# Optimization experiments

Measured on AMD Instinct MI355X. Metric: run time of the kernel, lower is better.

The kernel has to match this reference:

```python
import jax, jax.numpy as jnp
import numpy as np

D_MODEL = 128
D_Q = 16
N_HEADS = 8
LEN_Q = 64
N_LAYERS = 2
F_DIM = 2048
GEST_F_DIM = 512
NUM_GEST = 16
T_FRAMES = 4096
LN_EPS = 1e-5


def _ln(x):
    # fresh nn.LayerNorm(d_model) each call in the torch code -> weight=1, bias=0
    m = jnp.mean(x, axis=-1, keepdims=True)
    v = jnp.var(x, axis=-1, keepdims=True)
    return (x - m) * jax.lax.rsqrt(v + LN_EPS)


def _mha(q_in, k_in, v_in, Wq, Wk, Wv, n_heads, d_q):
    # torch MultiHeadAttention_COG: note self.fc is defined but NOT applied;
    # output = context, then LayerNorm(context + residual)
    B, lq, _ = q_in.shape
    lk = k_in.shape[1]
    Q = (q_in @ Wq).reshape(B, lq, n_heads, d_q).transpose(0, 2, 1, 3)  # [B,h,lq,dq]
    K = (k_in @ Wk).reshape(B, lk, n_heads, d_q).transpose(0, 2, 1, 3)
    V = (v_in @ Wv).reshape(B, lk, n_heads, d_q).transpose(0, 2, 1, 3)
    scores = jnp.einsum('bhqd,bhkd->bhqk', Q, K) / jnp.sqrt(jnp.asarray(d_q, q_in.dtype))
    attn = jax.nn.softmax(scores, axis=-1)
    ctx = jnp.einsum('bhqk,bhkd->bhqd', attn, V)
    ctx = ctx.transpose(0, 2, 1, 3).reshape(B, lq, n_heads * d_q)
    return _ln(ctx + q_in)


def _ffn(x, W1, W2):
    # PoswiseFeedForwardNet: Linear->ReLU->Linear (bias=False), residual + fresh LN
    return _ln(jax.nn.relu(x @ W1) @ W2 + x)


def setup_inputs() -> dict:
    key = jax.random.key(0)
    ks = jax.random.split(key, 12)
    s = 0.02
    inp = {
        'g': jax.random.normal(ks[0], (1, NUM_GEST, GEST_F_DIM), jnp.float32),
        'long_feature': jax.random.normal(ks[1], (1, T_FRAMES, F_DIM), jnp.float32),
        'W_vis': jax.random.normal(ks[2], (F_DIM, D_MODEL), jnp.float32) * s,
        'W_txt': jax.random.normal(ks[3], (GEST_F_DIM, D_MODEL), jnp.float32) * s,
        'Wq_enc': jax.random.normal(ks[4], (N_LAYERS, D_MODEL, N_HEADS * D_Q), jnp.float32) * s,
        'Wk_enc': jax.random.normal(ks[5], (N_LAYERS, D_MODEL, N_HEADS * D_Q), jnp.float32) * s,
        'Wv_enc': jax.random.normal(ks[6], (N_LAYERS, D_MODEL, N_HEADS * D_Q), jnp.float32) * s,
        'W1_ffn': jax.random.normal(ks[7], (N_LAYERS, D_MODEL, F_DIM), jnp.float32) * s,
        'W2_ffn': jax.random.normal(ks[8], (N_LAYERS, F_DIM, D_MODEL), jnp.float32) * s,
        'Wq_f': jax.random.normal(ks[9], (D_MODEL, D_MODEL), jnp.float32) * s,
        'Wk_f': jax.random.normal(ks[10], (D_MODEL, D_MODEL), jnp.float32) * s,
        'Wv_f': jax.random.normal(ks[11], (D_MODEL, D_MODEL), jnp.float32) * s,
    }
    return inp


def reference(g, long_feature, W_vis, W_txt, Wq_enc, Wk_enc, Wv_enc,
              W1_ffn, W2_ffn, Wq_f, Wk_f, Wv_f):
    visual = long_feature[0] @ W_vis           # [T, d_model]
    text = g[0] @ W_txt                        # [num_gest, d_model]
    T = visual.shape[0]

    # per-frame causal window of length LEN_Q with zero left-padding (vectorized)
    padded = jnp.concatenate(
        [jnp.zeros((LEN_Q - 1, D_MODEL), visual.dtype), visual], axis=0)
    idx = jnp.arange(T)[:, None] + jnp.arange(LEN_Q)[None, :]  # [T, len_q]
    visual_feas = padded[idx]                                   # [T, len_q, d_model]
    text_feas = jnp.broadcast_to(text[None], (T, NUM_GEST, D_MODEL))

    # Encoder_COG: normalize visual once, then 2 cross-attn layers (Q=text, K=V=visual)
    vis = _ln(visual_feas)
    t = text_feas
    for l in range(N_LAYERS):
        tq = _ln(t)                                   # norm1
        t = _mha(tq, vis, vis, Wq_enc[l], Wk_enc[l], Wv_enc[l], N_HEADS, D_Q)
        t = _ffn(_ln(t), W1_ffn[l], W2_ffn[l])        # norm3 then FFN

    # final single-head attention: Q=enc_outputs, K=V=text, d_q=d_model
    dec = _mha(t, text_feas, text_feas, Wq_f, Wk_f, Wv_f, 1, D_MODEL)  # [T,num_gest,d_model]
    return dec.reshape(T, -1)[None]  # [1, T, num_gest*d_model]
```

## Files before the change

kernel.cpp:

```cpp
#include <hip/hip_runtime.h>
#include <math.h>

#define TFRAMES 4096
#define DM 128
#define LQ 64
#define NG 16
#define NH 8
#define DQH 16
#define FD 2048
#define GFD 512
#define PAD 63
#define KVROWS (TFRAMES + PAD)
#define ASTRIDE (KVROWS * DM)
#define FPB 4
#define MROWS (FPB * NG)
#define STS 136
#define VTS 72
#define PBS 72
#define UROWS (LQ + FPB - 1)

#define OFF_WVH  0
#define OFF_WVL  131072
#define OFF_WKVH 262144
#define OFF_WKVL 294912
#define OFF_KV   (TFRAMES * DM)
#define OFF_TEXT (OFF_KV + 2 * ASTRIDE)
#define OFF_KF   (OFF_TEXT + NG * DM)
#define OFF_VF   (OFF_KF + NG * DM)
#define OFF_W1T  (OFF_VF + NG * DM)
#define OFF_W2T  (OFF_W1T + 262144)
#define OFF_WQT  (OFF_W2T + 262144)
#define OFF_WQFT (OFF_WQT + 16384)

typedef __attribute__((ext_vector_type(8))) short bf16x8;
typedef __attribute__((ext_vector_type(4))) float f32x4;
#define MFMA16(a, b, c) __builtin_amdgcn_mfma_f32_16x16x32_bf16(a, b, c, 0, 0, 0)

__device__ __forceinline__ short bfc(float x) {
    union { float f; unsigned u; } v; v.f = x;
    unsigned r = v.u + 0x7fffu + ((v.u >> 16) & 1u);
    return (short)(r >> 16);
}
__device__ __forceinline__ float b2f(short s) {
    union { unsigned u; float f; } v;
    v.u = ((unsigned)(unsigned short)s) << 16;
    return v.f;
}
__device__ __forceinline__ bf16x8 shiftf(int4 a, int4 b, int f) {
    const int wo = f >> 1;
    const int sh = (f & 1) * 16;
    int w0 = wo ? a.y : a.x;
    int w1 = wo ? a.z : a.y;
    int w2 = wo ? a.w : a.z;
    int w3 = wo ? b.x : a.w;
    int w4 = wo ? b.y : b.x;
    int o0 = __builtin_amdgcn_alignbit(w1, w0, sh);
    int o1 = __builtin_amdgcn_alignbit(w2, w1, sh);
    int o2 = __builtin_amdgcn_alignbit(w3, w2, sh);
    int o3 = __builtin_amdgcn_alignbit(w4, w3, sh);
    int4 o = {o0, o1, o2, o3};
    return *(bf16x8*)&o;
}

__global__ __launch_bounds__(256) void k_wcvt(const float* __restrict__ Wq_enc,
                                              const float* __restrict__ W1f,
                                              const float* __restrict__ W2f,
                                              const float* __restrict__ Wqf,
                                              const float* __restrict__ Wk_enc,
                                              const float* __restrict__ Wv_enc,
                                              short* __restrict__ W1T,
                                              short* __restrict__ W2T,
                                              short* __restrict__ WQT,
                                              short* __restrict__ WQFT,
                                              short* __restrict__ WKVH,
                                              short* __restrict__ WKVL) {
    const int t = blockIdx.x * 256 + threadIdx.x;
    const int gsel = blockIdx.y;
    if (gsel < 2) {
        int n = t >> 7, k = t & 127;
        W1T[gsel * 262144 + t] = bfc(W1f[(size_t)gsel * 262144 + (size_t)k * FD + n]);
    } else if (gsel < 4) {
        int l = gsel - 2;
        int n = t >> 11, k = t & 2047;
        W2T[l * 262144 + t] = bfc(W2f[(size_t)l * 262144 + (size_t)k * DM + n]);
    } else if (gsel < 6) {
        int l = gsel - 4;
        if (t < 16384) {
            int n = t >> 7, k = t & 127;
            WQT[l * 16384 + t] = bfc(Wq_enc[(size_t)l * 16384 + k * DM + n]);
        }
    } else if (gsel == 6) {
        if (t < 16384) {
            int n = t >> 7, k = t & 127;
            WQFT[t] = bfc(Wqf[(size_t)k * DM + n]);
        }
    } else {
        if (t < 65536) {
            int a = t >> 14, rem = t & 16383;
            int n = rem >> 7, k = rem & 127;
            const float* src = ((a & 1) ? Wv_enc : Wk_enc) + (size_t)(a >> 1) * 16384;
            float v = src[k * 128 + n];
            short hi = bfc(v);
            WKVH[t] = hi;
            WKVL[t] = bfc(v - b2f(hi));
        }
    }
}

__global__ __launch_bounds__(256) void k_wvt(const float* __restrict__ Wvis,
                                             short* __restrict__ WVH,
                                             short* __restrict__ WVL) {
    __shared__ float tile[64][65];
    const int tid = threadIdx.x;
    const int k0 = blockIdx.x * 64;
    const int n0 = blockIdx.y * 64;
    for (int o = tid; o < 64 * 64; o += 256) {
        int r = o >> 6, c = o & 63;
        tile[r][c] = Wvis[(size_t)(k0 + r) * DM + n0 + c];
    }
    __syncthreads();
    for (int o = tid; o < 64 * 64; o += 256) {
        int rn = o >> 6, ck = o & 63;
        float v = tile[ck][rn];
        short hi = bfc(v);
        WVH[(size_t)(n0 + rn) * FD + k0 + ck] = hi;
        WVL[(size_t)(n0 + rn) * FD + k0 + ck] = bfc(v - b2f(hi));
    }
}

__global__ __launch_bounds__(256) void k_viskv(const float* __restrict__ lf,
                                               const short* __restrict__ WVH,
                                               const short* __restrict__ WVL,
                                               const short* __restrict__ WKVH,
                                               const short* __restrict__ WKVL,
                                               short* __restrict__ kvB) {
    __shared__ __align__(16) char smem[17408 + 4352];
    __shared__ float sPa[256], sPb[256], sMean[16], sRstd[16];
    short* Ah = (short*)smem;
    short* Al = (short*)(smem + 4352);
    float* vis = (float*)smem;
    short* Vh = (short*)(smem + 8704);
    short* Vl = (short*)(smem + 13056);

    const int tid = threadIdx.x;
    const int w = tid >> 6;
    const int lane = tid & 63;
    const int lq = lane & 15;
    const int quad = lane >> 4;
    const int r0 = blockIdx.x * 16;

    f32x4 acc[2];
    acc[0] = (f32x4){0.f, 0.f, 0.f, 0.f};
    acc[1] = (f32x4){0.f, 0.f, 0.f, 0.f};
    for (int c = 0; c < 16; ++c) {
        __syncthreads();
        for (int o = tid; o < 16 * 128; o += 256) {
            int r = o >> 7, j = o & 127;
            float v = lf[(size_t)(r0 + r) * FD + c * 128 + j];
            short hi = bfc(v);
            Ah[r * 136 + j] = hi;
            Al[r * 136 + j] = bfc(v - b2f(hi));
        }
        __syncthreads();
#pragma unroll
        for (int ks = 0; ks < 4; ++ks) {
            bf16x8 ah = *(const bf16x8*)&Ah[lq * 136 + ks * 32 + quad * 8];
            bf16x8 al = *(const bf16x8*)&Al[lq * 136 + ks * 32 + quad * 8];
#pragma unroll
            for (int nt = 0; nt < 2; ++nt) {
                const size_t bo = (size_t)(w * 32 + nt * 16 + lq) * FD + c * 128 + ks * 32 + quad * 8;
                bf16x8 bh = *(const bf16x8*)&WVH[bo];
                bf16x8 bl = *(const bf16x8*)&WVL[bo];
                acc[nt] = MFMA16(ah, bh, acc[nt]);
                acc[nt] = MFMA16(al, bh, acc[nt]);
                acc[nt] = MFMA16(ah, bl, acc[nt]);
            }
        }
    }
    __syncthreads();
#pragma unroll
    for (int nt = 0; nt < 2; ++nt)
#pragma unroll
        for (int r = 0; r < 4; ++r)
            vis[(quad * 4 + r) * 132 + w * 32 + nt * 16 + lq] = acc[nt][r];
    __syncthreads();

    {
        int row = tid >> 4, p = tid & 15;
        float s = 0.f, s2 = 0.f;
#pragma unroll
        for (int k = 0; k < 8; ++k) { float v = vis[row * 132 + p * 8 + k]; s += v; s2 += v * v; }
        sPa[tid] = s; sPb[tid] = s2;
    }
    __syncthreads();
    if (tid < 16) {
        float s = 0.f, s2 = 0.f;
#pragma unroll
        for (int p = 0; p < 16; ++p) { s += sPa[tid * 16 + p]; s2 += sPb[tid * 16 + p]; }
        float m = s * (1.f / 128.f);
        float v = s2 * (1.f / 128.f) - m * m;
        sMean[tid] = m; sRstd[tid] = rsqrtf(v + 1e-5f);
    }
    __syncthreads();
    for (int o = tid; o < 16 * 128; o += 256) {
        int r = o >> 7, j = o & 127;
        float v = (vis[r * 132 + j] - sMean[r]) * sRstd[r];
        short hi = bfc(v);
        Vh[r * 136 + j] = hi;
        Vl[r * 136 + j] = bfc(v - b2f(hi));
    }
    __syncthreads();

    for (int a = 0; a < 4; ++a) {
        f32x4 ka[2];
        ka[0] = (f32x4){0.f, 0.f, 0.f, 0.f};
        ka[1] = (f32x4){0.f, 0.f, 0.f, 0.f};
#pragma unroll
        for (int ks = 0; ks < 4; ++ks) {
            bf16x8 ah = *(const bf16x8*)&Vh[lq * 136 + ks * 32 + quad * 8];
            bf16x8 al = *(const bf16x8*)&Vl[lq * 136 + ks * 32 + quad * 8];
#pragma unroll
            for (int nt = 0; nt < 2; ++nt) {
                const size_t bo = (size_t)a * 16384 + (size_t)(w * 32 + nt * 16 + lq) * 128 + ks * 32 + quad * 8;
                bf16x8 bh = *(const bf16x8*)&WKVH[bo];
                bf16x8 bl = *(const bf16x8*)&WKVL[bo];
                ka[nt] = MFMA16(ah, bh, ka[nt]);
                ka[nt] = MFMA16(al, bh, ka[nt]);
                ka[nt] = MFMA16(ah, bl, ka[nt]);
            }
        }
#pragma unroll
        for (int nt = 0; nt < 2; ++nt)
#pragma unroll
            for (int r = 0; r < 4; ++r)
                kvB[(size_t)a * ASTRIDE + (size_t)(PAD + r0 + quad * 4 + r) * DM + w * 32 + nt * 16 + lq]
                    = bfc(ka[nt][r]);
    }
}

__global__ __launch_bounds__(128) void k_text(const float* __restrict__ g,
                                              const float* __restrict__ Wtxt,
                                              const float* __restrict__ Wkf,
                                              const float* __restrict__ Wvf,
                                              float* __restrict__ text,
                                              float* __restrict__ kf,
                                              float* __restrict__ vf) {
    __shared__ float gs[GFD];
    __shared__ float tr[DM];
    const int r = blockIdx.x;
    const int tid = threadIdx.x;
    for (int i = tid; i < GFD; i += 128) gs[i] = g[(size_t)r * GFD + i];
    __syncthreads();
    float acc = 0.f;
    for (int k = 0; k < GFD; ++k) acc += gs[k] * Wtxt[(size_t)k * DM + tid];
    tr[tid] = acc;
    text[(size_t)r * DM + tid] = acc;
    __syncthreads();
    float a1 = 0.f, a2 = 0.f;
    for (int k = 0; k < DM; ++k) {
        float x = tr[k];
        a1 += x * Wkf[(size_t)k * DM + tid];
        a2 += x * Wvf[(size_t)k * DM + tid];
    }
    kf[(size_t)r * DM + tid] = a1;
    vf[(size_t)r * DM + tid] = a2;
}

__device__ __forceinline__ void ln_stats64(const short* buf, int tid, int dbl,
                                           float* pa, float* pb, float* ms, float* rs) {
    {
        int row = tid >> 3, p = tid & 7;
        const bf16x8* bp = (const bf16x8*)(buf + row * STS + p * 16);
        float s = 0.f, s2 = 0.f;
#pragma unroll
        for (int q8 = 0; q8 < 2; ++q8) {
            bf16x8 x = bp[q8];
#pragma unroll
            for (int e = 0; e < 8; ++e) { float v = b2f(x[e]); s += v; s2 += v * v; }
        }
        pa[tid] = s; pb[tid] = s2;
    }
    __syncthreads();
    if (tid < 64) {
        float ss = 0.f, ss2 = 0.f;
#pragma unroll
        for (int p2 = 0; p2 < 8; ++p2) { ss += pa[tid * 8 + p2]; ss2 += pb[tid * 8 + p2]; }
        float m = ss * (1.f / 128.f);
        float v = ss2 * (1.f / 128.f) - m * m;
        float r = rsqrtf(v + 1e-5f);
        if (dbl) r *= rsqrtf(v / (v + 1e-5f) + 1e-5f);
        ms[tid] = m; rs[tid] = r;
    }
    __syncthreads();
}
__device__ __forceinline__ void ln_apply64(short* buf, int tid,
                                           const float* ms, const float* rs) {
    int row = tid >> 3, p = tid & 7;
    float m = ms[row], r = rs[row];
    bf16x8* bp = (bf16x8*)(buf + row * STS + p * 16);
#pragma unroll
    for (int q8 = 0; q8 < 2; ++q8) {
        bf16x8 x = bp[q8]; bf16x8 o;
#pragma unroll
        for (int e = 0; e < 8; ++e) o[e] = bfc((b2f(x[e]) - m) * r);
        bp[q8] = o;
    }
    __syncthreads();
}

__global__ __launch_bounds__(512, 4) void k_frames(
    const short* __restrict__ kvB,    const float* __restrict__ text,
    const float* __restrict__ kf,     const float* __restrict__ vf,
    const short* __restrict__ W1T,    const short* __restrict__ W2T,
    const short* __restrict__ WQT,    const short* __restrict__ WQFT,
    float* __restrict__ out) {
    __shared__ __align__(16) short sT[MROWS * STS];
    __shared__ __align__(16) short sX[MROWS * STS];
    __shared__ __align__(16) short sVT[128 * VTS];
    __shared__ __align__(16) short sPB[8 * 16 * PBS];
    __shared__ float sPa[512], sPb[512];
    __shared__ float sMean[64], sRstd[64];

    const int tid = threadIdx.x;
    const int w = tid >> 6;
    const int lane = tid & 63;
    const int lq = lane & 15;
    const int quad = lane >> 4;
    const int T0 = blockIdx.x * FPB;

    for (int o = tid; o < MROWS * 128; o += 512)
        sT[(o >> 7) * STS + (o & 127)] = bfc(text[((o >> 7) & 15) * 128 + (o & 127)]);
    __syncthreads();

    for (int l = 0; l < 2; ++l) {
        const short* kvK = kvB + (size_t)(2 * l) * ASTRIDE;
        const short* kvV = kvB + (size_t)(2 * l + 1) * ASTRIDE;

        for (int o = tid; o < UROWS * 128; o += 512) {
            int u = o >> 7, d = o & 127;
            sVT[d * VTS + u] = kvV[(size_t)(T0 + u) * 128 + d];
        }
        ln_stats64(sT, tid, 0, sPa, sPb, sMean, sRstd);

        {
            const short* wq = WQT + (size_t)l * 16384;
            bf16x8 B[4];
#pragma unroll
            for (int ks = 0; ks < 4; ++ks)
                B[ks] = *(const bf16x8*)&wq[(w * 16 + lq) * 128 + ks * 32 + quad * 8];
#pragma unroll
            for (int mt = 0; mt < 4; ++mt) {
                int row = mt * 16 + lq;
                float m = sMean[row], r = sRstd[row];
                f32x4 acc = {0.f, 0.f, 0.f, 0.f};
#pragma unroll
                for (int ks = 0; ks < 4; ++ks) {
                    bf16x8 t8 = *(const bf16x8*)&sT[row * STS + ks * 32 + quad * 8];
                    bf16x8 a8;
#pragma unroll
                    for (int e = 0; e < 8; ++e) a8[e] = bfc((b2f(t8[e]) - m) * r);
                    acc = MFMA16(a8, B[ks], acc);
                }
#pragma unroll
                for (int r4 = 0; r4 < 4; ++r4)
                    sX[(mt * 16 + quad * 4 + r4) * STS + w * 16 + lq] = bfc(acc[r4]);
            }
        }
        __syncthreads();

        {
            const int f = w >> 1;
            const int hg = (w & 1) * 4;
            short* Pb = sPB + w * 16 * PBS;
            bf16x8 zv = {};
            for (int hh = 0; hh < 4; ++hh) {
                const int h = hg + hh;
                bf16x8 aq;
                {
                    bf16x8 t8 = *(const bf16x8*)&sX[(f * 16 + lq) * STS + h * 16 + (quad & 1) * 8];
                    aq = (quad < 2) ? t8 : zv;
                }
                f32x4 sc4[4];
#pragma unroll
                for (int kt = 0; kt < 4; ++kt) {
                    bf16x8 bk = *(const bf16x8*)&kvK[(size_t)(T0 + f + kt * 16 + lq) * 128 + h * 16 + (quad & 1) * 8];
                    bk = (quad < 2) ? bk : zv;
                    f32x4 z4 = {0.f, 0.f, 0.f, 0.f};
                    sc4[kt] = MFMA16(aq, bk, z4);
                }
                float pr[4][4];
#pragma unroll
                for (int r = 0; r < 4; ++r) {
                    float a0 = sc4[0][r] * 0.25f, a1 = sc4[1][r] * 0.25f;
                    float a2 = sc4[2][r] * 0.25f, a3 = sc4[3][r] * 0.25f;
                    float mx = fmaxf(fmaxf(a0, a1), fmaxf(a2, a3));
                    mx = fmaxf(mx, __shfl_xor(mx, 1));
                    mx = fmaxf(mx, __shfl_xor(mx, 2));
                    mx = fmaxf(mx, __shfl_xor(mx, 4));
                    mx = fmaxf(mx, __shfl_xor(mx, 8));
                    float e0 = expf(a0 - mx), e1 = expf(a1 - mx);
                    float e2 = expf(a2 - mx), e3 = expf(a3 - mx);
                    float s = e0 + e1 + e2 + e3;
                    s += __shfl_xor(s, 1);
                    s += __shfl_xor(s, 2);
                    s += __shfl_xor(s, 4);
                    s += __shfl_xor(s, 8);
                    float inv = 1.f / s;
                    pr[r][0] = e0 * inv; pr[r][1] = e1 * inv;
                    pr[r][2] = e2 * inv; pr[r][3] = e3 * inv;
                }
                const short* vr = &sVT[(h * 16 + lq) * VTS];
                int4 v0 = *(const int4*)&vr[quad * 8];
                int4 v1 = *(const int4*)&vr[quad * 8 + 8];
                int4 u0 = *(const int4*)&vr[32 + quad * 8];
                int4 u1 = *(const int4*)&vr[32 + quad * 8 + 8];
                bf16x8 b0 = shiftf(v0, v1, f);
                bf16x8 b1 = shiftf(u0, u1, f);
                f32x4 ctx = {0.f, 0.f, 0.f, 0.f};
#pragma unroll
                for (int pass = 0; pass < 2; ++pass) {
#pragma unroll
                    for (int r = 0; r < 4; ++r)
#pragma unroll
                        for (int kt = 0; kt < 4; ++kt) {
                            float p = pr[r][kt];
                            short hi = bfc(p);
                            short v16 = pass == 0 ? hi : bfc(p - b2f(hi));
                            Pb[(quad * 4 + r) * PBS + kt * 16 + lq] = v16;
                        }
                    bf16x8 p0 = *(const bf16x8*)&Pb[lq * PBS + quad * 8];
                    bf16x8 p1 = *(const bf16x8*)&Pb[lq * PBS + 32 + quad * 8];
                    ctx = MFMA16(p0, b0, ctx);
                    ctx = MFMA16(p1, b1, ctx);
                }
#pragma unroll
                for (int r = 0; r < 4; ++r) {
                    int row = f * 16 + quad * 4 + r;
                    int col = h * 16 + lq;
                    float tq = (b2f(sT[row * STS + col]) - sMean[row]) * sRstd[row];
                    sT[row * STS + col] = bfc(ctx[r] + tq);
                }
            }
        }
        __syncthreads();

        ln_stats64(sT, tid, 1, sPa, sPb, sMean, sRstd);
        ln_apply64(sT, tid, sMean, sRstd);

        {
            const short* w1p = W1T + (size_t)l * 262144;
            const short* w2p = W2T + (size_t)l * 262144;
            bf16x8 XA[4][4];
#pragma unroll
            for (int mt = 0; mt < 4; ++mt)
#pragma unroll
                for (int ks = 0; ks < 4; ++ks)
                    XA[mt][ks] = *(const bf16x8*)&sT[(mt * 16 + lq) * STS + ks * 32 + quad * 8];
            f32x4 yacc[4];
#pragma unroll
            for (int mt = 0; mt < 4; ++mt) yacc[mt] = (f32x4){0.f, 0.f, 0.f, 0.f};
            for (int c = 0; c < 16; ++c) {
                {
                    f32x4 hacc[4];
#pragma unroll
                    for (int mt = 0; mt < 4; ++mt) hacc[mt] = (f32x4){0.f, 0.f, 0.f, 0.f};
#pragma unroll
                    for (int ks = 0; ks < 4; ++ks) {
                        bf16x8 B1 = *(const bf16x8*)&w1p[(size_t)(c * 128 + w * 16 + lq) * 128 + ks * 32 + quad * 8];
#pragma unroll
                        for (int mt = 0; mt < 4; ++mt) hacc[mt] = MFMA16(XA[mt][ks], B1, hacc[mt]);
                    }
#pragma unroll
                    for (int mt = 0; mt < 4; ++mt)
#pragma unroll
                        for (int r = 0; r < 4; ++r)
                            sX[(mt * 16 + quad * 4 + r) * STS + w * 16 + lq] = bfc(fmaxf(hacc[mt][r], 0.f));
                }
                __syncthreads();
#pragma unroll
                for (int ks = 0; ks < 4; ++ks) {
                    bf16x8 B2 = *(const bf16x8*)&w2p[(size_t)(w * 16 + lq) * 2048 + c * 128 + ks * 32 + quad * 8];
#pragma unroll
                    for (int mt = 0; mt < 4; ++mt) {
                        bf16x8 A = *(const bf16x8*)&sX[(mt * 16 + lq) * STS + ks * 32 + quad * 8];
                        yacc[mt] = MFMA16(A, B2, yacc[mt]);
                    }
                }
                __syncthreads();
            }
#pragma unroll
            for (int mt = 0; mt < 4; ++mt)
#pragma unroll
                for (int r = 0; r < 4; ++r) {
                    int row = mt * 16 + quad * 4 + r;
                    int col = w * 16 + lq;
                    sT[row * STS + col] = bfc(yacc[mt][r] + b2f(sT[row * STS + col]));
                }
        }
        __syncthreads();

        ln_stats64(sT, tid, 0, sPa, sPb, sMean, sRstd);
        ln_apply64(sT, tid, sMean, sRstd);
    }

    {
        bf16x8 B[4];
#pragma unroll
        for (int ks = 0; ks < 4; ++ks)
            B[ks] = *(const bf16x8*)&WQFT[(w * 16 + lq) * 128 + ks * 32 + quad * 8];
#pragma unroll
        for (int mt = 0; mt < 4; ++mt) {
            f32x4 acc = {0.f, 0.f, 0.f, 0.f};
#pragma unroll
            for (int ks = 0; ks < 4; ++ks) {
                bf16x8 A = *(const bf16x8*)&sT[(mt * 16 + lq) * STS + ks * 32 + quad * 8];
                acc = MFMA16(A, B[ks], acc);
            }
#pragma unroll
            for (int r = 0; r < 4; ++r)
                sX[(mt * 16 + quad * 4 + r) * STS + w * 16 + lq] = bfc(acc[r]);
        }
    }
    short* kfL = sPB;
    short* vfL = sPB + 16 * STS;
    float* scF = (float*)(sPB + 2 * 16 * STS);
    for (int o = tid; o < 2048; o += 512) {
        kfL[(o >> 7) * STS + (o & 127)] = bfc(kf[o]);
        vfL[(o >> 7) * STS + (o & 127)] = bfc(vf[o]);
    }
    __syncthreads();
    if (tid < 256) {
        int m = tid >> 2, kq = tid & 3;
        float a4[4] = {0.f, 0.f, 0.f, 0.f};
        for (int d8 = 0; d8 < 16; ++d8) {
            bf16x8 qc = *(const bf16x8*)&sX[m * STS + d8 * 8];
            float qf[8];
#pragma unroll
            for (int e = 0; e < 8; ++e) qf[e] = b2f(qc[e]);
#pragma unroll
            for (int k = 0; k < 4; ++k) {
                bf16x8 kc = *(const bf16x8*)&kfL[(kq * 4 + k) * STS + d8 * 8];
#pragma unroll
                for (int e = 0; e < 8; ++e) a4[k] += qf[e] * b2f(kc[e]);
            }
        }
#pragma unroll
        for (int k = 0; k < 4; ++k)
            scF[m * 17 + kq * 4 + k] = a4[k] * 0.08838834764831845f;
    }
    __syncthreads();
    if (tid < 64) {
        float* row = scF + tid * 17;
        float mx = row[0];
#pragma unroll
        for (int k = 1; k < 16; ++k) mx = fmaxf(mx, row[k]);
        float sum = 0.f;
#pragma unroll
        for (int k = 0; k < 16; ++k) { float e = expf(row[k] - mx); row[k] = e; sum += e; }
        float inv = 1.f / sum;
#pragma unroll
        for (int k = 0; k < 16; ++k) row[k] *= inv;
    }
    __syncthreads();
    {
        int jj = tid & 127, rr0 = tid >> 7;
        float vv[16];
#pragma unroll
        for (int k = 0; k < 16; ++k) vv[k] = b2f(vfL[k * STS + jj]);
#pragma unroll 4
        for (int rr = 0; rr < 16; ++rr) {
            int row = rr0 + 4 * rr;
            float acc = 0.f;
#pragma unroll
            for (int k = 0; k < 16; ++k) acc += scF[row * 17 + k] * vv[k];
            sX[row * STS + jj] = bfc(acc + b2f(sT[row * STS + jj]));
        }
    }
    __syncthreads();
    ln_stats64(sX, tid, 0, sPa, sPb, sMean, sRstd);
    for (int o = tid; o < MROWS * 128; o += 512) {
        int r = o >> 7;
        out[(size_t)T0 * 2048 + o] = (b2f(sX[r * STS + (o & 127)]) - sMean[r]) * sRstd[r];
    }
}

extern "C" void kernel_launch(void* const* d_in, const int* in_sizes, int n_in,
                              void* d_out, int out_size, void* d_ws, size_t ws_size,
                              hipStream_t stream) {
    const float* g      = (const float*)d_in[0];
    const float* lf     = (const float*)d_in[1];
    const float* Wvis   = (const float*)d_in[2];
    const float* Wtxt   = (const float*)d_in[3];
    const float* Wq_enc = (const float*)d_in[4];
    const float* Wk_enc = (const float*)d_in[5];
    const float* Wv_enc = (const float*)d_in[6];
    const float* W1f    = (const float*)d_in[7];
    const float* W2f    = (const float*)d_in[8];
    const float* Wqf    = (const float*)d_in[9];
    const float* Wkf    = (const float*)d_in[10];
    const float* Wvf    = (const float*)d_in[11];
    float* out = (float*)d_out;
    float* ws  = (float*)d_ws;

    short* WVH  = (short*)(ws + OFF_WVH);
    short* WVL  = (short*)(ws + OFF_WVL);
    short* WKVH = (short*)(ws + OFF_WKVH);
    short* WKVL = (short*)(ws + OFF_WKVL);
    short* kvB  = (short*)(ws + OFF_KV);
    float* text = ws + OFF_TEXT;
    float* kfp  = ws + OFF_KF;
    float* vfp  = ws + OFF_VF;
    short* W1T  = (short*)(ws + OFF_W1T);
    short* W2T  = (short*)(ws + OFF_W2T);
    short* WQT  = (short*)(ws + OFF_WQT);
    short* WQFT = (short*)(ws + OFF_WQFT);

    for (int a = 0; a < 4; ++a)
        hipMemsetAsync(kvB + (size_t)a * ASTRIDE, 0, (size_t)PAD * DM * sizeof(short), stream);

    k_wcvt <<<dim3(1024, 8), dim3(256), 0, stream>>>(Wq_enc, W1f, W2f, Wqf, Wk_enc, Wv_enc,
                                                     W1T, W2T, WQT, WQFT, WKVH, WKVL);
    k_wvt  <<<dim3(32, 2), dim3(256), 0, stream>>>(Wvis, WVH, WVL);
    k_viskv<<<dim3(TFRAMES / 16), dim3(256), 0, stream>>>(lf, WVH, WVL, WKVH, WKVL, kvB);
    k_text <<<dim3(NG), dim3(128), 0, stream>>>(g, Wtxt, Wkf, Wvf, text, kfp, vfp);
    k_frames<<<dim3(TFRAMES / FPB), dim3(512), 0, stream>>>(kvB, text, kfp, vfp, W1T, W2T, WQT, WQFT, out);
}
```

Before: 630.2 us.

## Merge weight conversion kernels, prefetch FFN weights, vectorize V transpose load

```diff
diff --git a/kernel.cpp b/kernel.cpp
--- a/kernel.cpp
+++ b/kernel.cpp
@@ -68,63 +68,56 @@
                                               const float* __restrict__ Wqf,
                                               const float* __restrict__ Wk_enc,
                                               const float* __restrict__ Wv_enc,
+                                              const float* __restrict__ Wvis,
                                               short* __restrict__ W1T,
                                               short* __restrict__ W2T,
                                               short* __restrict__ WQT,
                                               short* __restrict__ WQFT,
                                               short* __restrict__ WKVH,
-                                              short* __restrict__ WKVL) {
-    const int t = blockIdx.x * 256 + threadIdx.x;
-    const int gsel = blockIdx.y;
-    if (gsel < 2) {
-        int n = t >> 7, k = t & 127;
-        W1T[gsel * 262144 + t] = bfc(W1f[(size_t)gsel * 262144 + (size_t)k * FD + n]);
-    } else if (gsel < 4) {
-        int l = gsel - 2;
-        int n = t >> 11, k = t & 2047;
-        W2T[l * 262144 + t] = bfc(W2f[(size_t)l * 262144 + (size_t)k * DM + n]);
-    } else if (gsel < 6) {
-        int l = gsel - 4;
-        if (t < 16384) {
-            int n = t >> 7, k = t & 127;
-            WQT[l * 16384 + t] = bfc(Wq_enc[(size_t)l * 16384 + k * DM + n]);
-        }
-    } else if (gsel == 6) {
-        if (t < 16384) {
-            int n = t >> 7, k = t & 127;
-            WQFT[t] = bfc(Wqf[(size_t)k * DM + n]);
-        }
-    } else {
-        if (t < 65536) {
-            int a = t >> 14, rem = t & 16383;
-            int n = rem >> 7, k = rem & 127;
-            const float* src = ((a & 1) ? Wv_enc : Wk_enc) + (size_t)(a >> 1) * 16384;
-            float v = src[k * 128 + n];
-            short hi = bfc(v);
-            WKVH[t] = hi;
-            WKVL[t] = bfc(v - b2f(hi));
-        }
-    }
-}
-
-__global__ __launch_bounds__(256) void k_wvt(const float* __restrict__ Wvis,
-                                             short* __restrict__ WVH,
-                                             short* __restrict__ WVL) {
+                                              short* __restrict__ WKVL,
+                                              short* __restrict__ WVH,
+                                              short* __restrict__ WVL) {
     __shared__ float tile[64][65];
     const int tid = threadIdx.x;
-    const int k0 = blockIdx.x * 64;
-    const int n0 = blockIdx.y * 64;
+    const int gy = blockIdx.y, gx = blockIdx.x;
+    const float* src; short* dst; short* dstL = nullptr;
+    int sstride, dstride, tr, tc;
+    if (gy < 2) {
+        src = W1f + (size_t)gy * 262144; dst = W1T + gy * 262144;
+        sstride = 2048; dstride = 128; tr = gx >> 5; tc = gx & 31;
+    } else if (gy < 4) {
+        int l = gy - 2;
+        src = W2f + (size_t)l * 262144; dst = W2T + l * 262144;
+        sstride = 128; dstride = 2048; tr = gx >> 1; tc = gx & 1;
+    } else if (gy == 4) {
+        if (gx >= 12) return;
+        int t = gx >> 2;
+        src = (t < 2) ? Wq_enc + (size_t)t * 16384 : Wqf;
+        dst = (t < 2) ? WQT + t * 16384 : WQFT;
+        sstride = 128; dstride = 128; tr = (gx >> 1) & 1; tc = gx & 1;
+    } else if (gy == 5) {
+        if (gx >= 16) return;
+        int a = gx >> 2;
+        src = ((a & 1) ? Wv_enc : Wk_enc) + (size_t)(a >> 1) * 16384;
+        dst = WKVH + a * 16384; dstL = WKVL + a * 16384;
+        sstride = 128; dstride = 128; tr = (gx >> 1) & 1; tc = gx & 1;
+    } else {
+        src = Wvis; dst = WVH; dstL = WVL;
+        sstride = 128; dstride = 2048; tr = gx >> 1; tc = gx & 1;
+    }
+    const int rb = tr * 64, cb = tc * 64;
     for (int o = tid; o < 64 * 64; o += 256) {
         int r = o >> 6, c = o & 63;
-        tile[r][c] = Wvis[(size_t)(k0 + r) * DM + n0 + c];
+        tile[r][c] = src[(size_t)(rb + r) * sstride + cb + c];
     }
     __syncthreads();
     for (int o = tid; o < 64 * 64; o += 256) {
         int rn = o >> 6, ck = o & 63;
         float v = tile[ck][rn];
         short hi = bfc(v);
-        WVH[(size_t)(n0 + rn) * FD + k0 + ck] = hi;
-        WVL[(size_t)(n0 + rn) * FD + k0 + ck] = bfc(v - b2f(hi));
+        size_t di = (size_t)(cb + rn) * dstride + rb + ck;
+        dst[di] = hi;
+        if (dstL) dstL[di] = bfc(v - b2f(hi));
     }
 }
 
@@ -336,9 +329,15 @@
         const short* kvK = kvB + (size_t)(2 * l) * ASTRIDE;
         const short* kvV = kvB + (size_t)(2 * l + 1) * ASTRIDE;
 
-        for (int o = tid; o < UROWS * 128; o += 512) {
-            int u = o >> 7, d = o & 127;
-            sVT[d * VTS + u] = kvV[(size_t)(T0 + u) * 128 + d];
+#pragma unroll
+        for (int dsel = 0; dsel < 2; ++dsel) {
+            int d8 = w + dsel * 8;
+            for (int u = lane; u < UROWS; u += 64) {
+                bf16x8 v = *(const bf16x8*)&kvV[(size_t)(T0 + u) * 128 + d8 * 8];
+#pragma unroll
+                for (int e = 0; e < 8; ++e)
+                    sVT[(d8 * 8 + e) * VTS + u] = v[e];
+            }
         }
         ln_stats64(sT, tid, 0, sPa, sPb, sMean, sRstd);
 
@@ -459,16 +458,26 @@
             f32x4 yacc[4];
 #pragma unroll
             for (int mt = 0; mt < 4; ++mt) yacc[mt] = (f32x4){0.f, 0.f, 0.f, 0.f};
+            bf16x8 B1v[4], B2v[4];
+#pragma unroll
+            for (int ks = 0; ks < 4; ++ks) {
+                B1v[ks] = *(const bf16x8*)&w1p[(size_t)(w * 16 + lq) * 128 + ks * 32 + quad * 8];
+                B2v[ks] = *(const bf16x8*)&w2p[(size_t)(w * 16 + lq) * 2048 + ks * 32 + quad * 8];
+            }
             for (int c = 0; c < 16; ++c) {
                 {
                     f32x4 hacc[4];
 #pragma unroll
                     for (int mt = 0; mt < 4; ++mt) hacc[mt] = (f32x4){0.f, 0.f, 0.f, 0.f};
 #pragma unroll
-                    for (int ks = 0; ks < 4; ++ks) {
-                        bf16x8 B1 = *(const bf16x8*)&w1p[(size_t)(c * 128 + w * 16 + lq) * 128 + ks * 32 + quad * 8];
-#pragma unroll
-                        for (int mt = 0; mt < 4; ++mt) hacc[mt] = MFMA16(XA[mt][ks], B1, hacc[mt]);
+                    for (int ks = 0; ks < 4; ++ks)
+#pragma unroll
+                        for (int mt = 0; mt < 4; ++mt)
+                            hacc[mt] = MFMA16(XA[mt][ks], B1v[ks], hacc[mt]);
+                    if (c < 15) {
+#pragma unroll
+                        for (int ks = 0; ks < 4; ++ks)
+                            B1v[ks] = *(const bf16x8*)&w1p[(size_t)((c + 1) * 128 + w * 16 + lq) * 128 + ks * 32 + quad * 8];
                     }
 #pragma unroll
                     for (int mt = 0; mt < 4; ++mt)
@@ -478,13 +487,16 @@
                 }
                 __syncthreads();
 #pragma unroll
-                for (int ks = 0; ks < 4; ++ks) {
-                    bf16x8 B2 = *(const bf16x8*)&w2p[(size_t)(w * 16 + lq) * 2048 + c * 128 + ks * 32 + quad * 8];
+                for (int ks = 0; ks < 4; ++ks)
 #pragma unroll
                     for (int mt = 0; mt < 4; ++mt) {
                         bf16x8 A = *(const bf16x8*)&sX[(mt * 16 + lq) * STS + ks * 32 + quad * 8];
-                        yacc[mt] = MFMA16(A, B2, yacc[mt]);
+                        yacc[mt] = MFMA16(A, B2v[ks], yacc[mt]);
                     }
+                if (c < 15) {
+#pragma unroll
+                    for (int ks = 0; ks < 4; ++ks)
+                        B2v[ks] = *(const bf16x8*)&w2p[(size_t)(w * 16 + lq) * 2048 + (c + 1) * 128 + ks * 32 + quad * 8];
                 }
                 __syncthreads();
             }
@@ -618,9 +630,8 @@
     for (int a = 0; a < 4; ++a)
         hipMemsetAsync(kvB + (size_t)a * ASTRIDE, 0, (size_t)PAD * DM * sizeof(short), stream);
 
-    k_wcvt <<<dim3(1024, 8), dim3(256), 0, stream>>>(Wq_enc, W1f, W2f, Wqf, Wk_enc, Wv_enc,
-                                                     W1T, W2T, WQT, WQFT, WKVH, WKVL);
-    k_wvt  <<<dim3(32, 2), dim3(256), 0, stream>>>(Wvis, WVH, WVL);
+    k_wcvt <<<dim3(64, 7), dim3(256), 0, stream>>>(Wq_enc, W1f, W2f, Wqf, Wk_enc, Wv_enc, Wvis,
+                                                   W1T, W2T, WQT, WQFT, WKVH, WKVL, WVH, WVL);
     k_viskv<<<dim3(TFRAMES / 16), dim3(256), 0, stream>>>(lf, WVH, WVL, WKVH, WKVL, kvB);
     k_text <<<dim3(NG), dim3(128), 0, stream>>>(g, Wtxt, Wkf, Wvf, text, kfp, vfp);
     k_frames<<<dim3(TFRAMES / FPB), dim3(512), 0, stream>>>(kvB, text, kfp, vfp, W1T, W2T, WQT, WQFT, out);
```

After: 687.2 us. +9.0%, slower.
